# Performance work log

Hardware: AMD Instinct MI355X
Metric: run time of the kernel (lower is better)

Reference implementation:

```python
import jax, jax.numpy as jnp
import numpy as np

T = 48; S = 48; H = 250; EMB = 300; VOCAB = 50000; NL = 5


def setup_inputs():
    key = jax.random.key(0)
    ks = jax.random.split(key, 32)
    def rn(k, shape, scale=0.05):
        return jax.random.normal(k, shape, dtype=jnp.float32) * scale
    return {
        "x1": jax.random.randint(ks[0], (T,), 0, VOCAB),
        "x2": jax.random.randint(ks[1], (S,), 0, VOCAB),
        "emb": rn(ks[2], (VOCAB, EMB), 1.0),
        "w_ih_f": rn(ks[3], (4 * H, EMB)),
        "w_hh_f": rn(ks[4], (4 * H, H)),
        "b_f": rn(ks[5], (4 * H,)),
        "w_ih_b": rn(ks[6], (4 * H, EMB)),
        "w_hh_b": rn(ks[7], (4 * H, H)),
        "b_b": rn(ks[8], (4 * H,)),
        "c1_w": rn(ks[9], (128, 13, 3, 3)),  "c1_b": rn(ks[10], (128,)),
        "c2_w": rn(ks[11], (164, 128, 3, 3)), "c2_b": rn(ks[12], (164,)),
        "c3_w": rn(ks[13], (192, 164, 3, 3)), "c3_b": rn(ks[14], (192,)),
        "c4_w": rn(ks[15], (192, 192, 3, 3)), "c4_b": rn(ks[16], (192,)),
        "c5_w": rn(ks[17], (128, 192, 3, 3)), "c5_b": rn(ks[18], (128,)),
        "dnn_w": rn(ks[19], (128, 128)), "dnn_b": rn(ks[20], (128,)),
        "out_w": rn(ks[21], (NL, 128)), "out_b": rn(ks[22], (NL,)),
    }


def _lstm_dir(xW, w_hh, b, reverse):
    # xW: [T, 4H] precomputed input projection
    def cell(carry, g_in):
        h, c = carry
        g = g_in + h @ w_hh.T + b
        i, f, gg, o = jnp.split(g, 4)
        i = jax.nn.sigmoid(i); f = jax.nn.sigmoid(f)
        gg = jnp.tanh(gg); o = jax.nn.sigmoid(o)
        c = f * c + i * gg
        h = o * jnp.tanh(c)
        return (h, c), h
    h0 = jnp.zeros((w_hh.shape[1],), xW.dtype)
    _, hs = jax.lax.scan(cell, (h0, h0), xW, reverse=reverse)
    return hs  # [T, H], aligned to input positions


def _bilstm(x, w_ih_f, w_hh_f, b_f, w_ih_b, w_hh_b, b_b):
    hf = _lstm_dir(x @ w_ih_f.T, w_hh_f, b_f, False)
    hb = _lstm_dir(x @ w_ih_b.T, w_hh_b, b_b, True)
    return jnp.stack([hf, hb], axis=1)  # [T, 2, H]


def _sim(a, b):
    # a:[T,D], b:[S,D] -> [3,T,S] channels (dot, cos, l2) -- fully batched
    dot = a @ b.T
    na = jnp.sqrt(jnp.sum(a * a, -1))
    nb = jnp.sqrt(jnp.sum(b * b, -1))
    cos = dot / (na[:, None] * nb[None, :] + 1e-8)
    d2 = jnp.maximum(na[:, None] ** 2 + nb[None, :] ** 2 - 2.0 * dot, 1e-12)
    l2 = jnp.sqrt(d2)
    return jnp.stack([dot, cos, l2], 0)


def _sim_cube(seq1, seq2):
    h1f, h1b = seq1[:, 0], seq1[:, 1]
    h2f, h2b = seq2[:, 0], seq2[:, 1]
    parts = [
        _sim(jnp.concatenate([h1f, h1b], -1), jnp.concatenate([h2f, h2b], -1)),
        _sim(h1f, h2f),
        _sim(h1b, h2b),
        _sim(h1f + h1b, h2f + h2b),
    ]
    pad = jnp.zeros((1, seq1.shape[0], seq2.shape[0]), seq1.dtype)  # channel 12
    return jnp.concatenate(parts + [pad], 0)  # [13, T, S]


def _greedy_select(plane):
    # greedy non-conflicting pair selection over top (T+S) entries
    t, s = plane.shape
    _, idx = jax.lax.top_k(plane.reshape(-1), t + s)
    def step(carry, i):
        s1, s2, m = carry
        p1 = i // t  # faithful to original (divides by len(s1tag))
        p2 = i % s
        ok = (s1[p1] + s2[p2]) == 0
        s1 = s1.at[p1].set(jnp.where(ok, 1, s1[p1]))
        s2 = s2.at[p2].set(jnp.where(ok, 1, s2[p2]))
        m = m.at[p1, p2].set(m[p1, p2] | ok)
        return (s1, s2, m), None
    init = (jnp.zeros(t, jnp.int32), jnp.zeros(s, jnp.int32), jnp.zeros((t, s), bool))
    (_, _, m), _ = jax.lax.scan(step, init, idx)
    return m


def _focus_cube(sc):
    sel = _greedy_select(sc[10]) | _greedy_select(sc[11])
    mask = jnp.where(sel[None], 1.0, 0.1).astype(sc.dtype)  # 0.1 base per VDPWI
    mask = mask.at[12].set(1.0)
    return mask * sc


def _convnet(x, c1_w, c1_b, c2_w, c2_b, c3_w, c3_b, c4_w, c4_b, c5_w, c5_b,
             dnn_w, dnn_b, out_w, out_b):
    def conv(x, w, b):
        y = jax.lax.conv_general_dilated(
            x, w, (1, 1), ((1, 1), (1, 1)),
            dimension_numbers=("NCHW", "OIHW", "NCHW"))
        return y + b[None, :, None, None]
    def pool(x, k, st):
        return jax.lax.reduce_window(
            x, -jnp.inf, jax.lax.max, (1, 1, k, k), (1, 1, st, st), "VALID")
    x = pool(jax.nn.relu(conv(x, c1_w, c1_b)), 2, 2)  # 48->24
    x = pool(jax.nn.relu(conv(x, c2_w, c2_b)), 2, 2)  # 24->12
    x = pool(jax.nn.relu(conv(x, c3_w, c3_b)), 2, 2)  # 12->6
    x = pool(jax.nn.relu(conv(x, c4_w, c4_b)), 2, 2)  # 6->3
    x = pool(jax.nn.relu(conv(x, c5_w, c5_b)), 3, 1)  # 3->1
    x = x.reshape(x.shape[0], -1)  # [1, 128]
    x = jax.nn.relu(x @ dnn_w.T + dnn_b)
    return x @ out_w.T + out_b


def reference(x1, x2, emb, w_ih_f, w_hh_f, b_f, w_ih_b, w_hh_b, b_b,
              c1_w, c1_b, c2_w, c2_b, c3_w, c3_b, c4_w, c4_b, c5_w, c5_b,
              dnn_w, dnn_b, out_w, out_b):
    e1 = emb[x1]  # [T, 300]
    e2 = emb[x2]  # [S, 300]
    seq1 = _bilstm(e1, w_ih_f, w_hh_f, b_f, w_ih_b, w_hh_b, b_b)
    seq2 = _bilstm(e2, w_ih_f, w_hh_f, b_f, w_ih_b, w_hh_b, b_b)
    sc = _sim_cube(seq1, seq2)        # [13, T, S]
    fc = _focus_cube(sc)
    logits = _convnet(fc[None], c1_w, c1_b, c2_w, c2_b, c3_w, c3_b,
                      c4_w, c4_b, c5_w, c5_b, dnn_w, dnn_b, out_w, out_b)
    return jax.nn.log_softmax(logits, axis=-1)
```

## Files before the change

### kernel.cpp

```cpp
#include <hip/hip_runtime.h>
#include <math.h>


typedef __attribute__((ext_vector_type(2))) _Float16 h2f;

#define OFF_XW    0
#define OFF_HS    192000
#define OFF_SC    240000
#define OFF_BUFA  269952
#define OFF_BUFB  343680
#define OFF_WIHT  367296
#define OFF_WPK   967296
#define OFF_SEL   1217296

__device__ __forceinline__ float sigf(float x) { return 1.f / (1.f + expf(-x)); }

#if __has_builtin(__builtin_amdgcn_fdot2)
__device__ __forceinline__ float dot2(h2f a, h2f b, float c) {
    return __builtin_amdgcn_fdot2(a, b, c, false);
}
#else
__device__ __forceinline__ float dot2(h2f a, h2f b, float c) {
    return c + (float)a.x * (float)b.x + (float)a.y * (float)b.y;
}
#endif

__global__ void transpose_wih_kernel(const float* __restrict__ wf, const float* __restrict__ wb,
                                     float* __restrict__ wT)
{
    __shared__ float tile[32][33];
    int dir = blockIdx.z;
    const float* w = dir ? wb : wf;

    int j = blockIdx.x * 32 + threadIdx.y;
    int k = blockIdx.y * 32 + threadIdx.x;
    if (j < 1000 && k < 300)
        tile[threadIdx.y][threadIdx.x] = w[(size_t)j * 300 + k];
    __syncthreads();

    int ko = blockIdx.y * 32 + threadIdx.y;
    int jo = blockIdx.x * 32 + threadIdx.x;
    if (ko < 300 && jo < 1000)
        wT[(size_t)dir * 300000 + (size_t)ko * 1000 + jo] = tile[threadIdx.x][threadIdx.y];
}

__global__ void pack_whh_kernel(const float* __restrict__ wf, const float* __restrict__ wb,
                                unsigned int* __restrict__ wpk)
{
    int dir = blockIdx.x / 1000;
    int j   = blockIdx.x % 1000;
    const float* w = (dir ? wb : wf) + (size_t)j * 250;
    int p = threadIdx.x;
    if (p < 125) {
        float2 v = *(const float2*)(w + 2 * p);
        h2f pv; pv.x = (_Float16)v.x; pv.y = (_Float16)v.y;
        wpk[(size_t)dir * 125000 + (size_t)p * 1000 + j] = *(unsigned int*)&pv;
    }
}

__global__ void embed_xw_kernel(const int* __restrict__ x1, const int* __restrict__ x2,
                                const float* __restrict__ emb, const float* __restrict__ wT,
                                const float* __restrict__ b_f, const float* __restrict__ b_b,
                                float* __restrict__ xW)
{
    int t = blockIdx.x % 48;
    int m = blockIdx.x / 48;
    const int* x = (m < 2) ? x1 : x2;
    const float* w = wT + (size_t)(m & 1) * 300000;
    const float* bias = (m & 1) ? b_b : b_f;

    __shared__ float e[300];
    int row = x[t];
    for (int k = threadIdx.x; k < 300; k += 512)
        e[k] = emb[(size_t)row * 300 + k];
    __syncthreads();

    int j0 = threadIdx.x;
    int j1 = threadIdx.x + 512;
    int j1c = j1 < 1000 ? j1 : 999;
    float a0 = 0.f, a1 = 0.f;
    #pragma unroll 4
    for (int k = 0; k < 300; ++k) {
        float ek = e[k];
        const float* wr = w + (size_t)k * 1000;
        a0 += ek * wr[j0];
        a1 += ek * wr[j1c];
    }
    float* out = xW + ((size_t)m * 48 + t) * 1000;
    out[j0] = a0 + bias[j0];
    if (j1 < 1000) out[j1] = a1 + bias[j1];
}

__global__ void __launch_bounds__(512, 1) lstm_kernel(
    const float* __restrict__ xW, const unsigned int* __restrict__ wpk,
    float* __restrict__ hs)
{
    int m   = blockIdx.x;
    int dir = m & 1;
    const unsigned int* wp = wpk + (size_t)dir * 125000;
    const float* xw = xW + (size_t)m * 48000;
    float* out      = hs + (size_t)m * 12000;

    int t = threadIdx.x;
    bool active = t < 500;
    int r0 = t, r1 = t + 500;

    __shared__ __align__(16) unsigned int hp[128];
    __shared__ float fo_lds[500];
    __shared__ unsigned int wl[12 * 1000];

    for (int idx = t; idx < 12000; idx += 512)
        wl[idx] = wp[idx];

    h2f w0r[113], w1r[113];
    if (active) {
        #pragma unroll
        for (int p = 0; p < 113; ++p) {
            unsigned int a = wp[(p + 12) * 1000 + r0];
            unsigned int b = wp[(p + 12) * 1000 + r1];
            w0r[p] = *(h2f*)&a;
            w1r[p] = *(h2f*)&b;
        }
    }
    if (t < 128) hp[t] = 0u;
    float c = 0.f;
    __syncthreads();

    for (int step = 0; step < 48; ++step) {
        int tt = dir ? 47 - step : step;
        float a0 = 0.f, a1 = 0.f;
        if (active) {
            const float* xwt = xw + tt * 1000;
            a0 = xwt[r0];
            a1 = xwt[r1];
            const uint4* hp4 = (const uint4*)hp;
            #pragma unroll
            for (int q = 0; q < 3; ++q) {
                uint4 hq = hp4[q];
                h2f h0 = *(h2f*)&hq.x, h1 = *(h2f*)&hq.y, h2v = *(h2f*)&hq.z, h3 = *(h2f*)&hq.w;
                unsigned int u00 = wl[(4 * q + 0) * 1000 + r0], u01 = wl[(4 * q + 0) * 1000 + r1];
                unsigned int u10 = wl[(4 * q + 1) * 1000 + r0], u11 = wl[(4 * q + 1) * 1000 + r1];
                unsigned int u20 = wl[(4 * q + 2) * 1000 + r0], u21 = wl[(4 * q + 2) * 1000 + r1];
                unsigned int u30 = wl[(4 * q + 3) * 1000 + r0], u31 = wl[(4 * q + 3) * 1000 + r1];
                a0 = dot2(*(h2f*)&u00, h0, a0);  a1 = dot2(*(h2f*)&u01, h0, a1);
                a0 = dot2(*(h2f*)&u10, h1, a0);  a1 = dot2(*(h2f*)&u11, h1, a1);
                a0 = dot2(*(h2f*)&u20, h2v, a0); a1 = dot2(*(h2f*)&u21, h2v, a1);
                a0 = dot2(*(h2f*)&u30, h3, a0);  a1 = dot2(*(h2f*)&u31, h3, a1);
            }
            #pragma unroll
            for (int jj = 3; jj < 31; ++jj) {
                uint4 hq = hp4[jj];
                h2f h0 = *(h2f*)&hq.x, h1 = *(h2f*)&hq.y, h2v = *(h2f*)&hq.z, h3 = *(h2f*)&hq.w;
                int p = 4 * jj - 12;
                a0 = dot2(w0r[p + 0], h0, a0);  a1 = dot2(w1r[p + 0], h0, a1);
                a0 = dot2(w0r[p + 1], h1, a0);  a1 = dot2(w1r[p + 1], h1, a1);
                a0 = dot2(w0r[p + 2], h2v, a0); a1 = dot2(w1r[p + 2], h2v, a1);
                a0 = dot2(w0r[p + 3], h3, a0);  a1 = dot2(w1r[p + 3], h3, a1);
            }
            {
                unsigned int hq = hp[124];
                h2f hv = *(h2f*)&hq;
                a0 = dot2(w0r[112], hv, a0);
                a1 = dot2(w1r[112], hv, a1);
            }
            if (t >= 250) {
                fo_lds[t - 250] = sigf(a0);
                fo_lds[250 + (t - 250)] = sigf(a1);
            }
        }
        __syncthreads();
        if (t < 250) {
            float iv = sigf(a0);
            float gv = tanhf(a1);
            float fv = fo_lds[t];
            float ov = fo_lds[250 + t];
            c = fv * c + iv * gv;
            float hn = ov * tanhf(c);
            out[tt * 250 + t] = hn;
            float hi = __shfl_down(hn, 1);
            if (!(t & 1)) {
                h2f pv; pv.x = (_Float16)hn; pv.y = (_Float16)hi;
                hp[t >> 1] = *(unsigned int*)&pv;
            }
        }
        __syncthreads();
    }
}

__global__ void sim_kernel(const float* __restrict__ hs, float* __restrict__ sc)
{
    int p = blockIdx.x;
    int i = p / 48, jj = p % 48;
    const float* h1f = hs + ((size_t)0 * 48 + i) * 250;
    const float* h1b = hs + ((size_t)1 * 48 + i) * 250;
    const float* h2f = hs + ((size_t)2 * 48 + jj) * 250;
    const float* h2b = hs + ((size_t)3 * 48 + jj) * 250;
    int lane = threadIdx.x;
    float dff = 0.f, dbb = 0.f, dfb = 0.f, dbf = 0.f;
    float sfa = 0.f, sba = 0.f, caa = 0.f;
    float sfb = 0.f, sbb = 0.f, cbb = 0.f;
    for (int k = lane; k < 250; k += 64) {
        float af = h1f[k], ab = h1b[k], bf = h2f[k], bb = h2b[k];
        dff += af * bf; dbb += ab * bb; dfb += af * bb; dbf += ab * bf;
        sfa += af * af; sba += ab * ab; caa += af * ab;
        sfb += bf * bf; sbb += bb * bb; cbb += bf * bb;
    }
    #pragma unroll
    for (int o = 32; o; o >>= 1) {
        dff += __shfl_down(dff, o); dbb += __shfl_down(dbb, o);
        dfb += __shfl_down(dfb, o); dbf += __shfl_down(dbf, o);
        sfa += __shfl_down(sfa, o); sba += __shfl_down(sba, o);
        caa += __shfl_down(caa, o);
        sfb += __shfl_down(sfb, o); sbb += __shfl_down(sbb, o);
        cbb += __shfl_down(cbb, o);
    }
    if (lane == 0) {
        #define EMIT(basep, dotv, sa2, sb2)                                 \
        {                                                                   \
            float na = sqrtf(sa2), nbv = sqrtf(sb2);                        \
            float dv = (dotv);                                              \
            sc[(basep) * 2304 + p] = dv;                                    \
            sc[((basep) + 1) * 2304 + p] = dv / (na * nbv + 1e-8f);         \
            float d2 = fmaxf(na * na + nbv * nbv - 2.f * dv, 1e-12f);       \
            sc[((basep) + 2) * 2304 + p] = sqrtf(d2);                       \
        }
        EMIT(0, dff + dbb, sfa + sba, sfb + sbb);
        EMIT(3, dff, sfa, sfb);
        EMIT(6, dbb, sba, sbb);
        EMIT(9, dff + dfb + dbf + dbb, sfa + sba + 2.f * caa, sfb + sbb + 2.f * cbb);
        #undef EMIT
    }
}

__global__ void greedy_kernel(const float* __restrict__ sc, unsigned char* __restrict__ sel)
{
    __shared__ float vals[2304];
    __shared__ int s1[48], s2[48];
    __shared__ unsigned char selL[2304];
    int lane = threadIdx.x;
    int plane = 10 + blockIdx.x;

    for (int q = 0; q < 36; ++q) {
        int i = lane + 64 * q;
        vals[i] = sc[plane * 2304 + i];
        selL[i] = 0;
    }
    if (lane < 48) { s1[lane] = 0; s2[lane] = 0; }
    __syncthreads();

    float lv = -INFINITY; int li = 0x7fffffff;
    for (int q = 0; q < 36; ++q) {
        int i = lane + 64 * q;
        float v = vals[i];
        if (v > lv) { lv = v; li = i; }
    }

    for (int it = 0; it < 96; ++it) {
        float bv = lv; int bi = li;
        #pragma unroll
        for (int o = 1; o < 64; o <<= 1) {
            float ov = __shfl_xor(bv, o);
            int   oi = __shfl_xor(bi, o);
            if (ov > bv || (ov == bv && oi < bi)) { bv = ov; bi = oi; }
        }
        if (lane == (bi & 63)) {
            vals[bi] = -INFINITY;
            lv = -INFINITY; li = 0x7fffffff;
            for (int q = 0; q < 36; ++q) {
                int i = lane + 64 * q;
                float v = vals[i];
                if (v > lv) { lv = v; li = i; }
            }
        }
        if (lane == 0) {
            int p1 = bi / 48, p2 = bi % 48;
            if (s1[p1] + s2[p2] == 0) { s1[p1] = 1; s2[p2] = 1; selL[bi] = 1; }
        }
    }
    __syncthreads();
    for (int q = 0; q < 36; ++q) {
        int i = lane + 64 * q;
        sel[blockIdx.x * 2304 + i] = selL[i];
    }
}

__global__ void conv1_pool_kernel(const float* __restrict__ sc, const unsigned char* __restrict__ sel,
                                  const float* __restrict__ w, const float* __restrict__ bias,
                                  float* __restrict__ out)
{
    __shared__ float tile[256];
    int co  = blockIdx.x / 9;
    int tl  = blockIdx.x % 9;
    int ty0 = (tl / 3) * 16, tx0 = (tl % 3) * 16;
    int tx = threadIdx.x % 16, ty = threadIdx.x / 16;
    int x = tx0 + tx, y = ty0 + ty;

    float mv[9];
    #pragma unroll
    for (int ky = 0; ky < 3; ++ky) {
        int iy = y + ky - 1;
        #pragma unroll
        for (int kx = 0; kx < 3; ++kx) {
            int ix = x + kx - 1;
            float mm = 0.f;
            if (iy >= 0 && iy < 48 && ix >= 0 && ix < 48) {
                int p = iy * 48 + ix;
                mm = (sel[p] | sel[2304 + p]) ? 1.0f : 0.1f;
            }
            mv[ky * 3 + kx] = mm;
        }
    }

    float acc = bias[co];
    const float* wco = w + (size_t)co * 13 * 9;
    for (int ci = 0; ci < 12; ++ci) {
        const float* inp = sc + (size_t)ci * 2304;
        const float* wp = wco + ci * 9;
        #pragma unroll
        for (int ky = 0; ky < 3; ++ky) {
            int iy = y + ky - 1;
            if (iy < 0 || iy >= 48) continue;
            #pragma unroll
            for (int kx = 0; kx < 3; ++kx) {
                int ix = x + kx - 1;
                if (ix < 0 || ix >= 48) continue;
                acc += inp[iy * 48 + ix] * mv[ky * 3 + kx] * wp[ky * 3 + kx];
            }
        }
    }
    tile[threadIdx.x] = acc > 0.f ? acc : 0.f;
    __syncthreads();
    if (threadIdx.x < 64) {
        int py = threadIdx.x / 8, px = threadIdx.x % 8;
        float a = tile[(py * 2) * 16 + px * 2];
        float b = tile[(py * 2) * 16 + px * 2 + 1];
        float cc = tile[(py * 2 + 1) * 16 + px * 2];
        float d = tile[(py * 2 + 1) * 16 + px * 2 + 1];
        float best = fmaxf(fmaxf(a, b), fmaxf(cc, d));
        out[(size_t)co * 576 + (ty0 / 2 + py) * 24 + (tx0 / 2 + px)] = best;
    }
}

__global__ void conv_cs_kernel(const float* __restrict__ in, const float* __restrict__ w,
                               const float* __restrict__ bias, float* __restrict__ out,
                               int Cin, int H, int W, int tileH, int tileW,
                               int cpc, int CC, int pk, int ps, int PHf, int PWf)
{
    extern __shared__ float sm[];
    int P = tileH * tileW;
    int co = blockIdx.x;
    int ty0 = blockIdx.y * tileH, tx0 = blockIdx.z * tileW;
    int t = threadIdx.x;
    int pix = t % P, chunk = t / P;
    int y = ty0 + pix / tileW, x = tx0 + pix % tileW;
    int c0 = chunk * cpc;
    int c1 = c0 + cpc; if (c1 > Cin) c1 = Cin;

    float acc = 0.f;
    const float* wco = w + (size_t)co * Cin * 9;
    for (int ci = c0; ci < c1; ++ci) {
        const float* inp = in + (size_t)ci * H * W;
        const float* wp = wco + (size_t)ci * 9;
        #pragma unroll
        for (int ky = 0; ky < 3; ++ky) {
            int iy = y + ky - 1;
            if (iy < 0 || iy >= H) continue;
            const float* rowp = inp + iy * W;
            #pragma unroll
            for (int kx = 0; kx < 3; ++kx) {
                int ix = x + kx - 1;
                if (ix < 0 || ix >= W) continue;
                acc += rowp[ix] * wp[ky * 3 + kx];
            }
        }
    }
    sm[t] = acc;
    __syncthreads();
    float* res = sm + P * CC;
    if (chunk == 0) {
        float tot = bias[co];
        for (int cc2 = 0; cc2 < CC; ++cc2) tot += sm[pix + cc2 * P];
        res[pix] = tot > 0.f ? tot : 0.f;
    }
    __syncthreads();
    int pH = (tileH - pk) / ps + 1, pW = (tileW - pk) / ps + 1;
    if (t < pH * pW) {
        int py = t / pW, px = t % pW;
        float best = -INFINITY;
        for (int dy = 0; dy < pk; ++dy)
            for (int dx = 0; dx < pk; ++dx) {
                float v = res[(py * ps + dy) * tileW + (px * ps + dx)];
                best = v > best ? v : best;
            }
        out[((size_t)co * PHf + (ty0 / ps + py)) * PWf + (tx0 / ps + px)] = best;
    }
}

__global__ void head_kernel(const float* __restrict__ feat,
                            const float* __restrict__ dnn_w, const float* __restrict__ dnn_b,
                            const float* __restrict__ out_w, const float* __restrict__ out_b,
                            float* __restrict__ out)
{
    __shared__ float y[128];
    __shared__ float logits[5];
    int j = threadIdx.x;
    float acc = dnn_b[j];
    for (int k = 0; k < 128; ++k) acc += feat[k] * dnn_w[j * 128 + k];
    y[j] = acc > 0.f ? acc : 0.f;
    __syncthreads();
    if (j < 5) {
        float a = out_b[j];
        for (int k = 0; k < 128; ++k) a += y[k] * out_w[j * 128 + k];
        logits[j] = a;
    }
    __syncthreads();
    if (j == 0) {
        float m = logits[0];
        for (int l = 1; l < 5; ++l) m = fmaxf(m, logits[l]);
        float s = 0.f;
        for (int l = 0; l < 5; ++l) s += expf(logits[l] - m);
        float lse = logf(s);
        for (int l = 0; l < 5; ++l) out[l] = logits[l] - m - lse;
    }
}

extern "C" void kernel_launch(void* const* d_in, const int* in_sizes, int n_in,
                              void* d_out, int out_size, void* d_ws, size_t ws_size,
                              hipStream_t stream)
{
    const int*   x1     = (const int*)d_in[0];
    const int*   x2     = (const int*)d_in[1];
    const float* emb    = (const float*)d_in[2];
    const float* w_ih_f = (const float*)d_in[3];
    const float* w_hh_f = (const float*)d_in[4];
    const float* b_f    = (const float*)d_in[5];
    const float* w_ih_b = (const float*)d_in[6];
    const float* w_hh_b = (const float*)d_in[7];
    const float* b_b    = (const float*)d_in[8];
    const float* c1_w   = (const float*)d_in[9];
    const float* c1_b   = (const float*)d_in[10];
    const float* c2_w   = (const float*)d_in[11];
    const float* c2_b   = (const float*)d_in[12];
    const float* c3_w   = (const float*)d_in[13];
    const float* c3_b   = (const float*)d_in[14];
    const float* c4_w   = (const float*)d_in[15];
    const float* c4_b   = (const float*)d_in[16];
    const float* c5_w   = (const float*)d_in[17];
    const float* c5_b   = (const float*)d_in[18];
    const float* dnn_w  = (const float*)d_in[19];
    const float* dnn_b  = (const float*)d_in[20];
    const float* out_w  = (const float*)d_in[21];
    const float* out_b  = (const float*)d_in[22];

    float* ws    = (float*)d_ws;
    float* xW    = ws + OFF_XW;
    float* hsb   = ws + OFF_HS;
    float* sc    = ws + OFF_SC;
    float* bufA  = ws + OFF_BUFA;
    float* bufB  = ws + OFF_BUFB;
    float* wihT  = ws + OFF_WIHT;
    unsigned int* wpk = (unsigned int*)(ws + OFF_WPK);
    unsigned char* sel = (unsigned char*)(ws + OFF_SEL);
    float* outp  = (float*)d_out;

    transpose_wih_kernel<<<dim3(32, 10, 2), dim3(32, 32), 0, stream>>>(w_ih_f, w_ih_b, wihT);
    pack_whh_kernel<<<2000, 128, 0, stream>>>(w_hh_f, w_hh_b, wpk);
    embed_xw_kernel<<<192, 512, 0, stream>>>(x1, x2, emb, wihT, b_f, b_b, xW);
    lstm_kernel<<<4, 512, 0, stream>>>(xW, wpk, hsb);
    sim_kernel<<<2304, 64, 0, stream>>>(hsb, sc);
    greedy_kernel<<<2, 64, 0, stream>>>(sc, sel);

    conv1_pool_kernel<<<128 * 9, 256, 0, stream>>>(sc, sel, c1_w, c1_b, bufA);
    conv_cs_kernel<<<dim3(164, 2, 2), 576, (576 + 144) * 4, stream>>>(
        bufA, c2_w, c2_b, bufB, 128, 24, 24, 12, 12, 32, 4, 2, 2, 12, 12);
    conv_cs_kernel<<<dim3(192, 1, 1), 576, (576 + 144) * 4, stream>>>(
        bufB, c3_w, c3_b, bufA, 164, 12, 12, 12, 12, 41, 4, 2, 2, 6, 6);
    conv_cs_kernel<<<dim3(192, 1, 1), 576, (576 + 36) * 4, stream>>>(
        bufA, c4_w, c4_b, bufB, 192, 6, 6, 6, 6, 12, 16, 2, 2, 3, 3);
    conv_cs_kernel<<<dim3(128, 1, 1), 576, (576 + 9) * 4, stream>>>(
        bufB, c5_w, c5_b, bufA, 192, 3, 3, 3, 3, 3, 64, 3, 1, 1, 1);

    head_kernel<<<1, 128, 0, stream>>>(bufA, dnn_w, dnn_b, out_w, out_b, outp);
}
```

Baseline: 390.4 us.

## Replace iterative greedy argmax with bitonic sort of packed keys

The greedy selection kernel used to run 96 sequential wave-wide argmax reductions, each followed by a single-lane rescan of 36 values. It now packs each value with its index into an order-preserving 64-bit key, bitonic-sorts 4096 keys in shared memory with 256 threads, and then walks the top 96 serially using row and column bitmasks. This removes the long serial dependency chain but adds 78 barrier-separated sort passes over a 32 KB shared array.

Measured after the change: 451.3 us. 15.6% more time.

```diff
diff --git a/kernel.cpp b/kernel.cpp
--- a/kernel.cpp
+++ b/kernel.cpp
@@ -3,6 +3,7 @@
 
 
 typedef __attribute__((ext_vector_type(2))) _Float16 h2f;
+typedef unsigned long long u64;
 
 #define OFF_XW    0
 #define OFF_HS    192000
@@ -234,54 +235,52 @@
 
 __global__ void greedy_kernel(const float* __restrict__ sc, unsigned char* __restrict__ sel)
 {
-    __shared__ float vals[2304];
-    __shared__ int s1[48], s2[48];
+    __shared__ u64 keys[4096];
     __shared__ unsigned char selL[2304];
-    int lane = threadIdx.x;
+    int tid = threadIdx.x;
     int plane = 10 + blockIdx.x;
 
-    for (int q = 0; q < 36; ++q) {
-        int i = lane + 64 * q;
-        vals[i] = sc[plane * 2304 + i];
-        selL[i] = 0;
-    }
-    if (lane < 48) { s1[lane] = 0; s2[lane] = 0; }
-    __syncthreads();
-
-    float lv = -INFINITY; int li = 0x7fffffff;
-    for (int q = 0; q < 36; ++q) {
-        int i = lane + 64 * q;
-        float v = vals[i];
-        if (v > lv) { lv = v; li = i; }
-    }
-
-    for (int it = 0; it < 96; ++it) {
-        float bv = lv; int bi = li;
-        #pragma unroll
-        for (int o = 1; o < 64; o <<= 1) {
-            float ov = __shfl_xor(bv, o);
-            int   oi = __shfl_xor(bi, o);
-            if (ov > bv || (ov == bv && oi < bi)) { bv = ov; bi = oi; }
-        }
-        if (lane == (bi & 63)) {
-            vals[bi] = -INFINITY;
-            lv = -INFINITY; li = 0x7fffffff;
-            for (int q = 0; q < 36; ++q) {
-                int i = lane + 64 * q;
-                float v = vals[i];
-                if (v > lv) { lv = v; li = i; }
-            }
-        }
-        if (lane == 0) {
-            int p1 = bi / 48, p2 = bi % 48;
-            if (s1[p1] + s2[p2] == 0) { s1[p1] = 1; s2[p2] = 1; selL[bi] = 1; }
-        }
-    }
-    __syncthreads();
-    for (int q = 0; q < 36; ++q) {
-        int i = lane + 64 * q;
+    for (int i = tid; i < 4096; i += 256) {
+        u64 key = 0;
+        if (i < 2304) {
+            unsigned int u = __float_as_uint(sc[plane * 2304 + i]);
+            unsigned int ord = (u & 0x80000000u) ? ~u : (u | 0x80000000u);
+            key = ((u64)ord << 32) | (unsigned int)(4095 - i);
+            selL[i] = 0;
+        }
+        keys[i] = key;
+    }
+    __syncthreads();
+
+    for (int k = 2; k <= 4096; k <<= 1) {
+        for (int j = k >> 1; j > 0; j >>= 1) {
+            for (int i = tid; i < 4096; i += 256) {
+                int ixj = i ^ j;
+                if (ixj > i) {
+                    u64 a = keys[i], b = keys[ixj];
+                    bool up = ((i & k) == 0);
+                    if (up ? (a < b) : (a > b)) { keys[i] = b; keys[ixj] = a; }
+                }
+            }
+            __syncthreads();
+        }
+    }
+
+    if (tid == 0) {
+        u64 m1 = 0, m2 = 0;
+        for (int q = 0; q < 96; ++q) {
+            int idx = 4095 - (int)(keys[q] & 0xFFFFFFFFu);
+            int p1 = idx / 48, p2 = idx % 48;
+            if (!((m1 >> p1) & 1) && !((m2 >> p2) & 1)) {
+                m1 |= 1ull << p1;
+                m2 |= 1ull << p2;
+                selL[idx] = 1;
+            }
+        }
+    }
+    __syncthreads();
+    for (int i = tid; i < 2304; i += 256)
         sel[blockIdx.x * 2304 + i] = selL[i];
-    }
 }
 
 __global__ void conv1_pool_kernel(const float* __restrict__ sc, const unsigned char* __restrict__ sel,
@@ -468,7 +467,7 @@
     embed_xw_kernel<<<192, 512, 0, stream>>>(x1, x2, emb, wihT, b_f, b_b, xW);
     lstm_kernel<<<4, 512, 0, stream>>>(xW, wpk, hsb);
     sim_kernel<<<2304, 64, 0, stream>>>(hsb, sc);
-    greedy_kernel<<<2, 64, 0, stream>>>(sc, sel);
+    greedy_kernel<<<2, 256, 0, stream>>>(sc, sel);
 
     conv1_pool_kernel<<<128 * 9, 256, 0, stream>>>(sc, sel, c1_w, c1_b, bufA);
     conv_cs_kernel<<<dim3(164, 2, 2), 576, (576 + 144) * 4, stream>>>(
```
